# Performance work log

Measured on AMD Instinct MI355X. Metric: run time of the kernel, lower is better.

## Reference

```python
import jax, jax.numpy as jnp
import numpy as np

B, S, D = 2, 2048, 2048
HQ, HKV, HD = 16, 8, 128
F = 8192
V = 32000
L = 2
SW = 512
SOFTCAP = 50.0
THETA = 10000.0
EPS = 1e-6
LAYER_TYPES = ("sliding_attention", "full_attention")
SCALE = HD ** -0.5


def _rms_norm(x, w):
    # Gemma-style RMSNorm: fp32 compute, (1 + weight) scale
    x32 = x.astype(jnp.float32)
    n = x32 * jax.lax.rsqrt(jnp.mean(x32 * x32, axis=-1, keepdims=True) + EPS)
    return (n * (1.0 + w.astype(jnp.float32))).astype(x.dtype)


def _rotate_half(x):
    x1, x2 = jnp.split(x, 2, axis=-1)
    return jnp.concatenate([-x2, x1], axis=-1)


def _rope_cos_sin(position_ids):
    inv_freq = 1.0 / (THETA ** (jnp.arange(0, HD, 2, dtype=jnp.float32) / HD))  # [HD/2]
    freqs = position_ids.astype(jnp.float32)[..., None] * inv_freq  # [B,S,HD/2]
    emb = jnp.concatenate([freqs, freqs], axis=-1)  # [B,S,HD]
    return jnp.cos(emb), jnp.sin(emb)


def _apply_rope(q, k, cos, sin):
    # q,k: [B,H,S,HD]; cos,sin: [B,S,HD] -> unsqueeze head dim
    c, s = cos[:, None], sin[:, None]
    return q * c + _rotate_half(q) * s, k * c + _rotate_half(k) * s


def _build_masks(attention_mask, position_ids):
    key_mask = attention_mask.astype(bool)  # [B,S]
    # segment ids from position resets (packed sequences)
    boundaries = (position_ids[:, 1:] <= position_ids[:, :-1]).astype(jnp.int32)
    seg = jnp.cumsum(jnp.concatenate([jnp.ones((B, 1), jnp.int32), boundaries], axis=1), axis=1)
    block = seg[:, :, None] == seg[:, None, :]  # [B,S,S]
    full = (key_mask[:, None, :] & block)[:, None]  # [B,1,S,S]
    rows = jnp.arange(S)
    dist = rows[:, None] - rows[None, :]
    left = (SW + 1) // 2
    right = SW // 2 + 1
    window = ((dist >= 0) & (dist < left)) | ((dist < 0) & (-dist < right))
    sliding = full & window[None, None]
    return {"full_attention": full, "sliding_attention": sliding}


def _attention(x, l, wq, wk, wv, wo, q_norm_w, k_norm_w, cos, sin, mask):
    q = jnp.einsum("bsd,dhe->bhse", x, wq[l].reshape(D, HQ, HD))
    k = jnp.einsum("bsd,dhe->bhse", x, wk[l].reshape(D, HKV, HD))
    v = jnp.einsum("bsd,dhe->bhse", x, wv[l].reshape(D, HKV, HD))
    q = _rms_norm(q, q_norm_w[l])
    k = _rms_norm(k, k_norm_w[l])
    q, k = _apply_rope(q, k, cos, sin)
    rep = HQ // HKV
    k = jnp.repeat(k, rep, axis=1)  # repeat_kv
    v = jnp.repeat(v, rep, axis=1)
    scores = jnp.einsum("bhqd,bhkd->bhqk", q, k) * SCALE
    scores = jnp.tanh(scores / SOFTCAP) * SOFTCAP  # logit softcapping
    big_neg = jnp.finfo(jnp.float32).min
    scores = jnp.where(mask, scores, big_neg)
    probs = jax.nn.softmax(scores.astype(jnp.float32), axis=-1).astype(x.dtype)
    out = jnp.einsum("bhqk,bhkd->bhqd", probs, v)
    out = out.transpose(0, 2, 1, 3).reshape(B, S, HQ * HD)
    return out @ wo[l]


def _mlp(x, l, w_gate_up, w_down):
    gu = x @ w_gate_up[l]
    gate, up = jnp.split(gu, 2, axis=-1)
    return (jax.nn.gelu(gate, approximate=True) * up) @ w_down[l]


def setup_inputs() -> dict:
    key = jax.random.key(0)
    ks = jax.random.split(key, 12)
    w = lambda k, shape: (jax.random.normal(k, shape, jnp.float32) * 0.02)
    inp = {
        "embed": w(ks[0], (V, D)),
        "wq": w(ks[1], (L, D, HQ * HD)),
        "wk": w(ks[2], (L, D, HKV * HD)),
        "wv": w(ks[3], (L, D, HKV * HD)),
        "wo": w(ks[4], (L, HQ * HD, D)),
        "q_norm_w": jnp.zeros((L, HD), jnp.float32),
        "k_norm_w": jnp.zeros((L, HD), jnp.float32),
        "ln_in": jnp.zeros((L, D), jnp.float32),
        "ln_post_attn": jnp.zeros((L, D), jnp.float32),
        "ln_pre_ffn": jnp.zeros((L, D), jnp.float32),
        "ln_post_ffn": jnp.zeros((L, D), jnp.float32),
        "w_gate_up": w(ks[5], (L, D, 2 * F)),
        "w_down": w(ks[6], (L, F, D)),
        "final_norm_w": jnp.zeros((D,), jnp.float32),
        "input_ids": jax.random.randint(ks[7], (B, S), 0, V, jnp.int32),
        "attention_mask": jnp.ones((B, S), jnp.int32),
        # packed sequences: positions reset at the midpoint of each row
        "position_ids": jnp.broadcast_to(
            jnp.concatenate([jnp.arange(S // 2), jnp.arange(S - S // 2)]).astype(jnp.int32)[None, :],
            (B, S),
        ),
    }
    return inp


def reference(embed, wq, wk, wv, wo, q_norm_w, k_norm_w, ln_in, ln_post_attn,
              ln_pre_ffn, ln_post_ffn, w_gate_up, w_down, final_norm_w,
              input_ids, attention_mask, position_ids):
    masks = _build_masks(attention_mask, position_ids)
    cos, sin = _rope_cos_sin(position_ids)
    # scaled word embedding (Gemma style)
    x = embed[input_ids] * jnp.asarray(D ** 0.5, embed.dtype)
    for l in range(L):
        mask = masks[LAYER_TYPES[l]]
        h = _rms_norm(x, ln_in[l])
        h = _attention(h, l, wq, wk, wv, wo, q_norm_w, k_norm_w, cos, sin, mask)
        x = x + _rms_norm(h, ln_post_attn[l])
        h = _rms_norm(x, ln_pre_ffn[l])
        h = _mlp(h, l, w_gate_up, w_down)
        x = x + _rms_norm(h, ln_post_ffn[l])
    return _rms_norm(x, final_norm_w)
```

## Files before the change

### kernel.cpp

```cpp
#include <hip/hip_runtime.h>
#include <cstdint>
#include <cstddef>

typedef __bf16 bf16x8 __attribute__((ext_vector_type(8)));
typedef float  f32x4  __attribute__((ext_vector_type(4)));

#define BATCH 2
#define SEQ   2048
#define DMODEL 2048
#define NHQ   16
#define NHKV  8
#define HDIM  128
#define FFDIM 8192
#define NTOK  4096

__device__ __forceinline__ f32x4 mfma16(bf16x8 a, bf16x8 b, f32x4 c) {
    return __builtin_amdgcn_mfma_f32_16x16x32_bf16(a, b, c, 0, 0, 0);
}

__device__ __forceinline__ void gload16(const __bf16* g, __bf16* l) {
    __builtin_amdgcn_global_load_lds(
        (const __attribute__((address_space(1))) void*)g,
        (__attribute__((address_space(3))) void*)l, 16, 0, 0);
}

__device__ inline float wave_sum64(float v) {
    v += __shfl_xor(v, 1);  v += __shfl_xor(v, 2);  v += __shfl_xor(v, 4);
    v += __shfl_xor(v, 8);  v += __shfl_xor(v, 16); v += __shfl_xor(v, 32);
    return v;
}

__device__ inline float block_sum256(float v, float* lds4) {
    v = wave_sum64(v);
    const int w = threadIdx.x >> 6;
    __syncthreads();
    if ((threadIdx.x & 63) == 0) lds4[w] = v;
    __syncthreads();
    return lds4[0] + lds4[1] + lds4[2] + lds4[3];
}

__device__ __forceinline__ float softcap_exp(float s_raw) {
    const float K1 = 0.08838834764831845f * 0.04f;
    float u = __expf(s_raw * K1);
    return __expf(50.f - 100.f * __builtin_amdgcn_rcpf(1.f + u));
}

__global__ void transpose_cvt(const float* __restrict__ src, __bf16* __restrict__ dst,
                              int K, int N) {
    __shared__ float tile[32][33];
    const int tx = threadIdx.x, ty = threadIdx.y;
    const int n0 = blockIdx.x * 32, k0 = blockIdx.y * 32;
    #pragma unroll
    for (int i = 0; i < 4; ++i)
        tile[ty + i * 8][tx] = src[(size_t)(k0 + ty + i * 8) * N + n0 + tx];
    __syncthreads();
    #pragma unroll
    for (int i = 0; i < 4; ++i)
        dst[(size_t)(n0 + ty + i * 8) * K + k0 + tx] = (__bf16)tile[tx][ty + i * 8];
}

__global__ void transpose_cvt_gu(const float* __restrict__ src, __bf16* __restrict__ dst,
                                 int K, int N) {
    __shared__ float tile[32][33];
    const int tx = threadIdx.x, ty = threadIdx.y;
    const int n0 = blockIdx.x * 32, k0 = blockIdx.y * 32;
    #pragma unroll
    for (int i = 0; i < 4; ++i)
        tile[ty + i * 8][tx] = src[(size_t)(k0 + ty + i * 8) * N + n0 + tx];
    __syncthreads();
    #pragma unroll
    for (int i = 0; i < 4; ++i) {
        int n = n0 + ty + i * 8;
        int rI;
        if (n < 8192) rI = ((n & ~15) << 1) + (n & 15);
        else { int u = n - 8192; rI = ((u & ~15) << 1) + 16 + (u & 15); }
        dst[(size_t)rI * K + k0 + tx] = (__bf16)tile[tx][ty + i * 8];
    }
}

__global__ void transpose_bf16_k(const __bf16* __restrict__ src0, __bf16* __restrict__ dst0,
                                 int R, int C) {
    __shared__ __bf16 tile[32][34];
    const int z = blockIdx.z;
    const __bf16* src = src0 + (size_t)z * R * C;
    __bf16* dst = dst0 + (size_t)z * R * C;
    const int tx = threadIdx.x, ty = threadIdx.y;
    const int c0 = blockIdx.x * 32, r0 = blockIdx.y * 32;
    #pragma unroll
    for (int i = 0; i < 4; ++i)
        tile[ty + i * 8][tx] = src[(size_t)(r0 + ty + i * 8) * C + c0 + tx];
    __syncthreads();
    #pragma unroll
    for (int i = 0; i < 4; ++i)
        dst[(size_t)(c0 + ty + i * 8) * R + r0 + tx] = tile[tx][ty + i * 8];
}

__global__ __launch_bounds__(256) void embed_k(const float* __restrict__ emb,
                                               const int* __restrict__ ids,
                                               float* __restrict__ x) {
    const int row = blockIdx.x, t = threadIdx.x;
    const int id = ids[row];
    const size_t src = (size_t)id * DMODEL, dst = (size_t)row * DMODEL;
    const float sc = 45.2548339959390f;
    float4 a = *(const float4*)&emb[src + t * 4];
    float4 b = *(const float4*)&emb[src + t * 4 + 1024];
    a.x *= sc; a.y *= sc; a.z *= sc; a.w *= sc;
    b.x *= sc; b.y *= sc; b.z *= sc; b.w *= sc;
    *(float4*)&x[dst + t * 4] = a;
    *(float4*)&x[dst + t * 4 + 1024] = b;
}

__global__ __launch_bounds__(256) void seg_scan(const int* __restrict__ pos,
                                                int* __restrict__ seg) {
    __shared__ int wsum[4];
    const int b = blockIdx.x, t = threadIdx.x;
    const int lane = t & 63, wv = t >> 6;
    const int base = b * SEQ;
    int f[8]; int loc = 0;
    #pragma unroll
    for (int i = 0; i < 8; ++i) {
        int s = t * 8 + i;
        int fl = (s > 0) ? (pos[base + s] <= pos[base + s - 1]) : 0;
        f[i] = fl; loc += fl;
    }
    int sc = loc;
    for (int o = 1; o < 64; o <<= 1) { int n = __shfl_up(sc, o); if (lane >= o) sc += n; }
    if (lane == 63) wsum[wv] = sc;
    __syncthreads();
    int wb = 0;
    for (int i = 0; i < wv; ++i) wb += wsum[i];
    int run = wb + sc - loc + 1;
    #pragma unroll
    for (int i = 0; i < 8; ++i) { run += f[i]; seg[base + t * 8 + i] = run; }
}

template<int MODE, int NH>
__global__ __launch_bounds__(256) void fused_norm_k(
        float* __restrict__ x, const float* __restrict__ hA, const float* __restrict__ hB,
        const float* __restrict__ wA, const float* __restrict__ wB,
        __bf16* __restrict__ outb, float* __restrict__ outf) {
    __shared__ float lds4[4];
    const int row = blockIdx.x, t = threadIdx.x;
    const size_t base = (size_t)row * DMODEL;
    const int c0 = t * 4, c1 = t * 4 + 1024;
    float v[8];
    if constexpr (MODE == 0) {
        float4 a = *(const float4*)&x[base + c0];
        float4 b = *(const float4*)&x[base + c1];
        v[0]=a.x; v[1]=a.y; v[2]=a.z; v[3]=a.w;
        v[4]=b.x; v[5]=b.y; v[6]=b.z; v[7]=b.w;
    } else {
        float4 ha = *(const float4*)&hA[base + c0];
        float4 hb = *(const float4*)&hA[base + c1];
        float hv[8] = {ha.x, ha.y, ha.z, ha.w, hb.x, hb.y, hb.z, hb.w};
        if constexpr (NH == 2) {
            float4 ga = *(const float4*)&hB[base + c0];
            float4 gb = *(const float4*)&hB[base + c1];
            hv[0]+=ga.x; hv[1]+=ga.y; hv[2]+=ga.z; hv[3]+=ga.w;
            hv[4]+=gb.x; hv[5]+=gb.y; hv[6]+=gb.z; hv[7]+=gb.w;
        }
        float ss = 0.f;
        #pragma unroll
        for (int i = 0; i < 8; ++i) ss += hv[i] * hv[i];
        float tot = block_sum256(ss, lds4);
        float rs = rsqrtf(tot * (1.f / DMODEL) + 1e-6f);
        float4 xa = *(const float4*)&x[base + c0];
        float4 xb = *(const float4*)&x[base + c1];
        float xv[8] = {xa.x, xa.y, xa.z, xa.w, xb.x, xb.y, xb.z, xb.w};
        #pragma unroll
        for (int i = 0; i < 8; ++i) {
            int c = (i < 4) ? c0 + i : c1 + i - 4;
            v[i] = xv[i] + hv[i] * rs * (1.f + wA[c]);
        }
        float4 o0 = {v[0], v[1], v[2], v[3]}, o1 = {v[4], v[5], v[6], v[7]};
        *(float4*)&x[base + c0] = o0;
        *(float4*)&x[base + c1] = o1;
    }
    float ss2 = 0.f;
    #pragma unroll
    for (int i = 0; i < 8; ++i) ss2 += v[i] * v[i];
    float tot2 = block_sum256(ss2, lds4);
    float rs2 = rsqrtf(tot2 * (1.f / DMODEL) + 1e-6f);
    #pragma unroll
    for (int i = 0; i < 8; ++i) {
        int c = (i < 4) ? c0 + i : c1 + i - 4;
        float o = v[i] * rs2 * (1.f + wB[c]);
        if constexpr (MODE == 2) outf[base + c] = o;
        else outb[base + c] = (__bf16)o;
    }
}

template<int MH, int NH>
__device__ __forceinline__ void quad(f32x4 (&acc)[8][4], const bf16x8 (&af)[4][2],
                                     const bf16x8 (&bfr)[2][2]) {
    #pragma unroll
    for (int mq = 0; mq < 4; ++mq)
        #pragma unroll
        for (int nq = 0; nq < 2; ++nq)
            #pragma unroll
            for (int ks = 0; ks < 2; ++ks)
                acc[MH*4+mq][NH*2+nq] = mfma16(af[mq][ks], bfr[nq][ks], acc[MH*4+mq][NH*2+nq]);
}

template<typename OutT, int GELU>
__global__ __launch_bounds__(512, 2) void gemm8p(const __bf16* __restrict__ A,
                                                 const __bf16* __restrict__ Bw,
                                                 OutT* __restrict__ C,
                                                 int M, int N, int Ksub, int lda, int ldb) {
    __shared__ __bf16 lds[65536];
    const int z = blockIdx.z;
    A += (size_t)z * Ksub;
    Bw += (size_t)z * Ksub;
    C += (size_t)z * M * N;

    const int nx = gridDim.x;
    const int ny = gridDim.y;
    const int nwg = nx * ny;
    const int orig = blockIdx.y * nx + blockIdx.x;
    const int wg = ((nwg & 7) == 0) ? ((orig & 7) * (nwg >> 3) + (orig >> 3)) : orig;
    const int gsize = 8 * nx;
    const int gid = wg / gsize;
    const int first_m = gid * 8;
    const int rows = min(8, ny - first_m);
    const int loc = wg - gid * gsize;
    const int bm = (first_m + loc % rows) * 256;
    const int bn = (loc / rows) * 256;

    const int t = threadIdx.x;
    const int w = t >> 6, lane = t & 63;
    const int wm = w >> 2, wn = w & 3;
    const int lg = lane >> 4, lr = lane & 15;

    const int rS = t >> 3, sS = t & 7;
    const int colS = ((sS ^ (rS & 7)) << 3);
    const __bf16* Ag = A + (size_t)(bm + rS) * lda + colS;
    const __bf16* Bg = Bw + (size_t)(bn + rS) * ldb + colS;
    const int nt = Ksub >> 6;

#define STAGE_AU(kt, h, s) { \
        const __bf16* g_ = Ag + (size_t)((h) * 128 + (s) * 64) * lda + (size_t)(kt) * 64; \
        gload16(g_, &lds[(((kt) & 1) << 15) + (h) * 8192 + (s) * 4096 + t * 8]); }
#define STAGE_BU(kt, h, s) { \
        const __bf16* g_ = Bg + (size_t)((h) * 128 + (s) * 64) * ldb + (size_t)(kt) * 64; \
        gload16(g_, &lds[(((kt) & 1) << 15) + 16384 + (h) * 8192 + (s) * 4096 + t * 8]); }

    f32x4 acc[8][4] = {};
    bf16x8 af[4][2], bf0[2][2], bf1[2][2];

    const int swz = (lr & 7) << 3;
    const int aBase = wm * 8192;
    const int bBase = 16384 + (wn >> 1) * 8192;
    const int bRow0 = (wn & 1) * 64;
    const int lo0 = (lg * 8) ^ swz;
    const int lo1 = (32 + lg * 8) ^ swz;

#define RD_A(bufv, rowoff) { \
        _Pragma("unroll") \
        for (int mq = 0; mq < 4; ++mq) { \
            const int rb_ = (bufv) + aBase + ((rowoff) + mq * 16 + lr) * 64; \
            af[mq][0] = *(const bf16x8*)&lds[rb_ + lo0]; \
            af[mq][1] = *(const bf16x8*)&lds[rb_ + lo1]; } }
#define RD_B0(bufv) { \
        _Pragma("unroll") \
        for (int nq = 0; nq < 2; ++nq) { \
            const int rb_ = (bufv) + bBase + (bRow0 + nq * 16 + lr) * 64; \
            bf0[nq][0] = *(const bf16x8*)&lds[rb_ + lo0]; \
            bf0[nq][1] = *(const bf16x8*)&lds[rb_ + lo1]; } }
#define RD_B1(bufv) { \
        _Pragma("unroll") \
        for (int nq = 0; nq < 2; ++nq) { \
            const int rb_ = (bufv) + bBase + (bRow0 + 32 + nq * 16 + lr) * 64; \
            bf1[nq][0] = *(const bf16x8*)&lds[rb_ + lo0]; \
            bf1[nq][1] = *(const bf16x8*)&lds[rb_ + lo1]; } }

    STAGE_BU(0, 0, 0); STAGE_BU(0, 0, 1); STAGE_BU(0, 1, 0); STAGE_BU(0, 1, 1);
    STAGE_AU(0, 0, 0); STAGE_AU(0, 1, 0); STAGE_AU(0, 0, 1); STAGE_AU(0, 1, 1);

    for (int kt = 0; kt < nt; ++kt) {
        const int buf = (kt & 1) << 15;
        const bool p1 = (kt + 1 < nt);
        if (p1) {
            STAGE_BU(kt + 1, 0, 0); STAGE_BU(kt + 1, 0, 1);
            asm volatile("s_waitcnt vmcnt(4)" ::: "memory");
        } else {
            asm volatile("s_waitcnt vmcnt(2)" ::: "memory");
        }
        __builtin_amdgcn_s_barrier();
        asm volatile("" ::: "memory");
        RD_A(buf, 0); RD_B0(buf);
        asm volatile("s_waitcnt lgkmcnt(0)" ::: "memory");
        __builtin_amdgcn_sched_barrier(0);
        __builtin_amdgcn_s_setprio(1);
        quad<0,0>(acc, af, bf0);
        __builtin_amdgcn_s_setprio(0);
        asm volatile("" ::: "memory");
        if (p1) { STAGE_BU(kt + 1, 1, 0); STAGE_BU(kt + 1, 1, 1); }
        RD_B1(buf);
        asm volatile("s_waitcnt lgkmcnt(0)" ::: "memory");
        __builtin_amdgcn_sched_barrier(0);
        __builtin_amdgcn_s_setprio(1);
        quad<0,1>(acc, af, bf1);
        __builtin_amdgcn_s_setprio(0);
        asm volatile("" ::: "memory");
        if (p1) {
            STAGE_AU(kt + 1, 0, 0); STAGE_AU(kt + 1, 1, 0);
            asm volatile("s_waitcnt vmcnt(6)" ::: "memory");
        } else {
            asm volatile("s_waitcnt vmcnt(0)" ::: "memory");
        }
        __builtin_amdgcn_s_barrier();
        asm volatile("" ::: "memory");
        RD_A(buf, 64);
        asm volatile("s_waitcnt lgkmcnt(0)" ::: "memory");
        __builtin_amdgcn_sched_barrier(0);
        __builtin_amdgcn_s_setprio(1);
        quad<1,1>(acc, af, bf1);
        __builtin_amdgcn_s_setprio(0);
        asm volatile("" ::: "memory");
        if (p1) { STAGE_AU(kt + 1, 0, 1); STAGE_AU(kt + 1, 1, 1); }
        __builtin_amdgcn_sched_barrier(0);
        __builtin_amdgcn_s_setprio(1);
        quad<1,0>(acc, af, bf0);
        __builtin_amdgcn_s_setprio(0);
        asm volatile("" ::: "memory");
    }
#undef STAGE_AU
#undef STAGE_BU
#undef RD_A
#undef RD_B0
#undef RD_B1

    if constexpr (GELU) {
        const int nhalf = N >> 1;
        #pragma unroll
        for (int m = 0; m < 8; ++m)
            #pragma unroll
            for (int pp = 0; pp < 2; ++pp)
                #pragma unroll
                for (int r = 0; r < 4; ++r) {
                    float g = acc[m][2 * pp][r];
                    float u = acc[m][2 * pp + 1][r];
                    float a2 = 1.5957691216057308f * (g + 0.044715f * g * g * g);
                    float sig = __builtin_amdgcn_rcpf(1.f + __expf(-a2));
                    float res = g * sig * u;
                    const int row = bm + wm * 128 + m * 16 + lg * 4 + r;
                    const int col = (bn >> 1) + wn * 32 + pp * 16 + lr;
                    C[(size_t)row * nhalf + col] = (OutT)res;
                }
    } else {
        #pragma unroll
        for (int m = 0; m < 8; ++m)
            #pragma unroll
            for (int n = 0; n < 4; ++n)
                #pragma unroll
                for (int r = 0; r < 4; ++r) {
                    const int row = bm + wm * 128 + m * 16 + lg * 4 + r;
                    const int col = bn + wn * 64 + n * 16 + lr;
                    C[(size_t)row * N + col] = (OutT)acc[m][n][r];
                }
    }
}

__global__ __launch_bounds__(256) void qkv_post(const __bf16* __restrict__ qkv,
                                                const float* __restrict__ qnw,
                                                const float* __restrict__ knw,
                                                const int* __restrict__ posid,
                                                __bf16* __restrict__ qg,
                                                __bf16* __restrict__ kg,
                                                __bf16* __restrict__ vg) {
    const int slot = blockIdx.x * 4 + (threadIdx.x >> 6);
    const int lane = threadIdx.x & 63;
    const int token = slot >> 5, j = slot & 31;
    const int b = token >> 11, s = token & (SEQ - 1);
    int base;
    const float* nw = nullptr;
    if (j < 16)      { base = j * 128;                nw = qnw; }
    else if (j < 24) { base = 2048 + (j - 16) * 128;  nw = knw; }
    else             { base = 3072 + (j - 24) * 128; }
    float e0 = (float)qkv[(size_t)token * 4096 + base + lane];
    float e1 = (float)qkv[(size_t)token * 4096 + base + lane + 64];
    if (j < 24) {
        float ss = wave_sum64(e0 * e0 + e1 * e1);
        float rs = rsqrtf(ss * (1.f / 128.f) + 1e-6f);
        e0 *= rs * (1.f + nw[lane]);
        e1 *= rs * (1.f + nw[lane + 64]);
        float p = (float)posid[token];
        float inv = exp2f(-13.287712379549449f * ((float)lane * (1.f / 64.f)));
        float f = p * inv;
        float c = cosf(f), sn = sinf(f);
        float o0 = e0 * c - e1 * sn;
        float o1 = e1 * c + e0 * sn;
        e0 = o0; e1 = o1;
    }
    size_t dst; __bf16* out;
    if (j < 16)      { dst = ((size_t)(b * NHQ  + j)        * SEQ + s) * HDIM; out = qg; }
    else if (j < 24) { dst = ((size_t)(b * NHKV + (j - 16)) * SEQ + s) * HDIM; out = kg; }
    else             { dst = ((size_t)(b * NHKV + (j - 24)) * SEQ + s) * HDIM; out = vg; }
    out[dst + lane] = (__bf16)e0;
    out[dst + lane + 64] = (__bf16)e1;
}

template<int SLIDING>
__global__ __launch_bounds__(256, 2) void attn_k(const __bf16* __restrict__ qg,
                                                 const __bf16* __restrict__ kg,
                                                 const __bf16* __restrict__ vtg,
                                                 const int* __restrict__ seg,
                                                 const int* __restrict__ amask,
                                                 __bf16* __restrict__ outg) {
    __shared__ __align__(16) __bf16 Ks[64][136];
    __shared__ __align__(16) __bf16 Vs[128][72];
    __shared__ __align__(16) __bf16 Ps[4][16][72];
    __shared__ int segq_s[64], segk_s[64], kmk_s[64];
    __shared__ int flag_s;
    const int bh = blockIdx.y;
    const int b = bh >> 4, h = bh & 15, kvh = h >> 1;
    const int qb = blockIdx.x * 64;
    const int t = threadIdx.x, w = t >> 6, lane = t & 63;
    const int lg = lane >> 4, lr = lane & 15;
    const int segbase = b * SEQ;

    const size_t qoff = ((size_t)(b * NHQ + h) * SEQ + qb + w * 16) * HDIM;
    bf16x8 qf[4];
    #pragma unroll
    for (int kk = 0; kk < 4; ++kk)
        qf[kk] = *(const bf16x8*)&qg[qoff + (size_t)lr * HDIM + kk * 32 + lg * 8];
    if (t < 64) segq_s[t] = seg[segbase + qb + t];

    const int sqmin = seg[segbase + qb], sqmax = seg[segbase + qb + 63];

    const int krow = t >> 4, kcol = (t & 15) * 8;
    const int vrow = t >> 3, vcol = (t & 7) * 8;
    const __bf16* kB = kg + ((size_t)(b * NHKV + kvh) * SEQ) * HDIM + (size_t)krow * HDIM + kcol;
    const __bf16* vB = vtg + ((size_t)(b * NHKV + kvh) * HDIM + vrow) * SEQ + vcol;

    auto chunk_active = [&](int kb) -> bool {
        if (SLIDING && (qb - kb < -318 || qb - kb > 319)) return false;
        int skmin = seg[segbase + kb], skmax = seg[segbase + kb + 63];
        return (skmax >= sqmin) && (skmin <= sqmax);
    };
    auto next_kb = [&](int kb) -> int {
        for (kb += 64; kb < SEQ; kb += 64)
            if (chunk_active(kb)) return kb;
        return SEQ;
    };

    int4 kr0, kr1, kr2, kr3, vr0, vr1, vr2, vr3;
#define LOADR(kb_) { \
        kr0 = *(const int4*)(kB + (size_t)(kb_) * HDIM); \
        kr1 = *(const int4*)(kB + (size_t)((kb_) + 16) * HDIM); \
        kr2 = *(const int4*)(kB + (size_t)((kb_) + 32) * HDIM); \
        kr3 = *(const int4*)(kB + (size_t)((kb_) + 48) * HDIM); \
        vr0 = *(const int4*)(vB + (kb_)); \
        vr1 = *(const int4*)(vB + (size_t)32 * SEQ + (kb_)); \
        vr2 = *(const int4*)(vB + (size_t)64 * SEQ + (kb_)); \
        vr3 = *(const int4*)(vB + (size_t)96 * SEQ + (kb_)); }

    f32x4 oacc[8] = {};
    float den[4] = {0.f, 0.f, 0.f, 0.f};

    int kb = chunk_active(0) ? 0 : next_kb(0);
    if (kb < SEQ) LOADR(kb);

    while (kb < SEQ) {
        const int nkb = next_kb(kb);
        __syncthreads();
        *(int4*)&Ks[krow     ][kcol] = kr0;
        *(int4*)&Ks[krow + 16][kcol] = kr1;
        *(int4*)&Ks[krow + 32][kcol] = kr2;
        *(int4*)&Ks[krow + 48][kcol] = kr3;
        *(int4*)&Vs[vrow     ][vcol] = vr0;
        *(int4*)&Vs[vrow + 32][vcol] = vr1;
        *(int4*)&Vs[vrow + 64][vcol] = vr2;
        *(int4*)&Vs[vrow + 96][vcol] = vr3;
        if (w == 0) {
            int m = amask[segbase + kb + lane];
            int sk = seg[segbase + kb + lane];
            kmk_s[lane] = m; segk_s[lane] = sk;
            bool allm = (__ballot(m != 0) == ~0ull);
            bool segu = __all(sk == sqmin) && (sqmin == sqmax);
            bool wall = !SLIDING || (qb - kb >= -193 && qb - kb <= 192);
            if (lane == 0) flag_s = (allm && segu && wall) ? 1 : 0;
        }
        __syncthreads();
        if (nkb < SEQ) LOADR(nkb);
        const bool fast = (flag_s != 0);

        #pragma unroll
        for (int n = 0; n < 4; ++n) {
            f32x4 sc = {};
            #pragma unroll
            for (int kk = 0; kk < 4; ++kk) {
                bf16x8 bfr = *(const bf16x8*)&Ks[n * 16 + lr][kk * 32 + lg * 8];
                sc = mfma16(qf[kk], bfr, sc);
            }
            if (fast) {
                #pragma unroll
                for (int r = 0; r < 4; ++r) {
                    int row = lg * 4 + r;
                    float p = softcap_exp(sc[r]);
                    den[r] += p;
                    Ps[w][row][n * 16 + lr] = (__bf16)p;
                }
            } else {
                #pragma unroll
                for (int r = 0; r < 4; ++r) {
                    int row = lg * 4 + r;
                    int qi = qb + w * 16 + row;
                    int ki = kb + n * 16 + lr;
                    bool ok = (kmk_s[n * 16 + lr] != 0) &&
                              (segq_s[w * 16 + row] == segk_s[n * 16 + lr]);
                    if (SLIDING) { int d = qi - ki; ok = ok && (d >= -256) && (d <= 255); }
                    float p = ok ? softcap_exp(sc[r]) : 0.f;
                    den[r] += p;
                    Ps[w][row][n * 16 + lr] = (__bf16)p;
                }
            }
        }
        #pragma unroll
        for (int kk2 = 0; kk2 < 2; ++kk2) {
            bf16x8 pf = *(const bf16x8*)&Ps[w][lr][kk2 * 32 + lg * 8];
            #pragma unroll
            for (int n2 = 0; n2 < 8; ++n2) {
                bf16x8 vf = *(const bf16x8*)&Vs[n2 * 16 + lr][kk2 * 32 + lg * 8];
                oacc[n2] = mfma16(pf, vf, oacc[n2]);
            }
        }
        kb = nkb;
    }
#undef LOADR
    #pragma unroll
    for (int r = 0; r < 4; ++r) {
        float v = den[r];
        v += __shfl_xor(v, 1); v += __shfl_xor(v, 2);
        v += __shfl_xor(v, 4); v += __shfl_xor(v, 8);
        den[r] = __builtin_amdgcn_rcpf(v);
    }
    #pragma unroll
    for (int n2 = 0; n2 < 8; ++n2)
        #pragma unroll
        for (int r = 0; r < 4; ++r) {
            int row = qb + w * 16 + lg * 4 + r;
            float val = oacc[n2][r] * den[r];
            outg[((size_t)(b * SEQ) + row) * DMODEL + h * HDIM + n2 * 16 + lr] = (__bf16)val;
        }
}

extern "C" void kernel_launch(void* const* d_in, const int* in_sizes, int n_in,
                              void* d_out, int out_size, void* d_ws, size_t ws_size,
                              hipStream_t stream) {
    const float* embedw = (const float*)d_in[0];
    const float* wq   = (const float*)d_in[1];
    const float* wk   = (const float*)d_in[2];
    const float* wv   = (const float*)d_in[3];
    const float* wo   = (const float*)d_in[4];
    const float* qnw  = (const float*)d_in[5];
    const float* knw  = (const float*)d_in[6];
    const float* lnin = (const float*)d_in[7];
    const float* lnpa = (const float*)d_in[8];
    const float* lnpf = (const float*)d_in[9];
    const float* lnpff= (const float*)d_in[10];
    const float* wguW = (const float*)d_in[11];
    const float* wdnW = (const float*)d_in[12];
    const float* fnw  = (const float*)d_in[13];
    const int* ids    = (const int*)d_in[14];
    const int* amask  = (const int*)d_in[15];
    const int* posid  = (const int*)d_in[16];
    float* outp = (float*)d_out;

    char* ws = (char*)d_ws;
    size_t off = 0;
    auto A = [&](size_t b) -> char* {
        char* p = ws + off;
        off = (off + b + 255) & ~(size_t)255;
        return p;
    };
    __bf16* qkvwt = (__bf16*)A((size_t)4096 * 2048 * 2);
    __bf16* wot   = (__bf16*)A((size_t)2048 * 2048 * 2);
    __bf16* wgut  = (__bf16*)A((size_t)16384 * 2048 * 2);
    __bf16* wdnt  = (__bf16*)A((size_t)2048 * 8192 * 2);
    float*  x     = (float*)A((size_t)NTOK * DMODEL * 4);
    __bf16* hbuf  = (__bf16*)A((size_t)NTOK * DMODEL * 2);
    __bf16* qkvb  = (__bf16*)A((size_t)NTOK * 4096 * 2);
    __bf16* qbh   = (__bf16*)A((size_t)BATCH * NHQ  * SEQ * HDIM * 2);
    __bf16* kbh   = (__bf16*)A((size_t)BATCH * NHKV * SEQ * HDIM * 2);
    __bf16* vbh   = (__bf16*)A((size_t)BATCH * NHKV * SEQ * HDIM * 2);
    __bf16* vtbh  = (__bf16*)A((size_t)BATCH * NHKV * SEQ * HDIM * 2);
    __bf16* attnb = (__bf16*)A((size_t)NTOK * DMODEL * 2);
    __bf16* actb  = (__bf16*)A((size_t)NTOK * FFDIM * 2);
    float*  pbuf  = (float*)A((size_t)2 * NTOK * DMODEL * 4);
    int*    seg   = (int*)A((size_t)BATCH * SEQ * 4);
    if (off > ws_size) return;

    const dim3 tb(32, 8);
    seg_scan<<<BATCH, 256, 0, stream>>>(posid, seg);
    embed_k<<<NTOK, 256, 0, stream>>>(embedw, ids, x);
    fused_norm_k<0,1><<<NTOK, 256, 0, stream>>>(x, nullptr, nullptr, nullptr, lnin, hbuf, nullptr);

    for (int l = 0; l < 2; ++l) {
        transpose_cvt<<<dim3(64, 64), tb, 0, stream>>>(wq + (size_t)l * 2048 * 2048,
            qkvwt, 2048, 2048);
        transpose_cvt<<<dim3(32, 64), tb, 0, stream>>>(wk + (size_t)l * 2048 * 1024,
            qkvwt + (size_t)2048 * 2048, 2048, 1024);
        transpose_cvt<<<dim3(32, 64), tb, 0, stream>>>(wv + (size_t)l * 2048 * 1024,
            qkvwt + (size_t)3072 * 2048, 2048, 1024);
        transpose_cvt<<<dim3(64, 64), tb, 0, stream>>>(wo + (size_t)l * 2048 * 2048,
            wot, 2048, 2048);
        transpose_cvt_gu<<<dim3(512, 64), tb, 0, stream>>>(wguW + (size_t)l * 2048 * 16384,
            wgut, 2048, 16384);
        transpose_cvt<<<dim3(64, 256), tb, 0, stream>>>(wdnW + (size_t)l * 8192 * 2048,
            wdnt, 8192, 2048);

        gemm8p<__bf16,0><<<dim3(16, 16, 1), 512, 0, stream>>>(hbuf, qkvwt, qkvb,
                                                              4096, 4096, 2048, 2048, 2048);
        qkv_post<<<32768, 256, 0, stream>>>(qkvb, qnw + l * 128, knw + l * 128, posid,
                                            qbh, kbh, vbh);
        transpose_bf16_k<<<dim3(4, 64, BATCH * NHKV), tb, 0, stream>>>(vbh, vtbh, SEQ, HDIM);
        if (l == 0)
            attn_k<1><<<dim3(SEQ / 64, BATCH * NHQ), 256, 0, stream>>>(qbh, kbh, vtbh, seg,
                                                                       amask, attnb);
        else
            attn_k<0><<<dim3(SEQ / 64, BATCH * NHQ), 256, 0, stream>>>(qbh, kbh, vtbh, seg,
                                                                       amask, attnb);
        gemm8p<float,0><<<dim3(8, 16, 2), 512, 0, stream>>>(attnb, wot, pbuf,
                                                            4096, 2048, 1024, 2048, 2048);
        fused_norm_k<1,2><<<NTOK, 256, 0, stream>>>(x, pbuf, pbuf + (size_t)NTOK * DMODEL,
                                                    lnpa + l * 2048, lnpf + l * 2048,
                                                    hbuf, nullptr);
        gemm8p<__bf16,1><<<dim3(64, 16, 1), 512, 0, stream>>>(hbuf, wgut, actb,
                                                              4096, 16384, 2048, 2048, 2048);
        gemm8p<float,0><<<dim3(8, 16, 2), 512, 0, stream>>>(actb, wdnt, pbuf,
                                                            4096, 2048, 4096, 8192, 8192);
        if (l == 0)
            fused_norm_k<1,2><<<NTOK, 256, 0, stream>>>(x, pbuf, pbuf + (size_t)NTOK * DMODEL,
                                                        lnpff, lnin + 2048, hbuf, nullptr);
        else
            fused_norm_k<2,2><<<NTOK, 256, 0, stream>>>(x, pbuf, pbuf + (size_t)NTOK * DMODEL,
                                                        lnpff + 2048, fnw, nullptr, outp);
    }
}
```

Measured before the change: 1.419 ms.

## Store split-K GEMM partials in bf16, raise attention occupancy, add MFMA priority

The split-K output-projection and down-projection GEMMs now write their two partial sums as bf16 instead of fp32. The fused norm kernel is templated to read bf16 partials, which halves the partial-buffer traffic. Separately, the attention kernel's launch bounds go from 2 to 3 blocks per SIMD, and s_setprio brackets are placed around its MFMA loops. The bf16 partials lose precision before the residual add, and the tighter launch bound may force register spills.

```diff
diff --git a/kernel.cpp b/kernel.cpp
--- a/kernel.cpp
+++ b/kernel.cpp
@@ -3,6 +3,7 @@
 #include <cstddef>
 
 typedef __bf16 bf16x8 __attribute__((ext_vector_type(8)));
+typedef __bf16 bf16x4 __attribute__((ext_vector_type(4)));
 typedef float  f32x4  __attribute__((ext_vector_type(4)));
 
 #define BATCH 2
@@ -43,6 +44,15 @@
     const float K1 = 0.08838834764831845f * 0.04f;
     float u = __expf(s_raw * K1);
     return __expf(50.f - 100.f * __builtin_amdgcn_rcpf(1.f + u));
+}
+
+__device__ __forceinline__ void ld4f(const float* p, float v[4]) {
+    float4 a = *(const float4*)p;
+    v[0] = a.x; v[1] = a.y; v[2] = a.z; v[3] = a.w;
+}
+__device__ __forceinline__ void ld4f(const __bf16* p, float v[4]) {
+    bf16x4 a = *(const bf16x4*)p;
+    v[0] = (float)a[0]; v[1] = (float)a[1]; v[2] = (float)a[2]; v[3] = (float)a[3];
 }
 
 __global__ void transpose_cvt(const float* __restrict__ src, __bf16* __restrict__ dst,
@@ -134,9 +144,9 @@
     for (int i = 0; i < 8; ++i) { run += f[i]; seg[base + t * 8 + i] = run; }
 }
 
-template<int MODE, int NH>
+template<int MODE, int NH, typename HT>
 __global__ __launch_bounds__(256) void fused_norm_k(
-        float* __restrict__ x, const float* __restrict__ hA, const float* __restrict__ hB,
+        float* __restrict__ x, const HT* __restrict__ hA, const HT* __restrict__ hB,
         const float* __restrict__ wA, const float* __restrict__ wB,
         __bf16* __restrict__ outb, float* __restrict__ outf) {
     __shared__ float lds4[4];
@@ -150,14 +160,15 @@
         v[0]=a.x; v[1]=a.y; v[2]=a.z; v[3]=a.w;
         v[4]=b.x; v[5]=b.y; v[6]=b.z; v[7]=b.w;
     } else {
-        float4 ha = *(const float4*)&hA[base + c0];
-        float4 hb = *(const float4*)&hA[base + c1];
-        float hv[8] = {ha.x, ha.y, ha.z, ha.w, hb.x, hb.y, hb.z, hb.w};
+        float hv[8];
+        ld4f(hA + base + c0, &hv[0]);
+        ld4f(hA + base + c1, &hv[4]);
         if constexpr (NH == 2) {
-            float4 ga = *(const float4*)&hB[base + c0];
-            float4 gb = *(const float4*)&hB[base + c1];
-            hv[0]+=ga.x; hv[1]+=ga.y; hv[2]+=ga.z; hv[3]+=ga.w;
-            hv[4]+=gb.x; hv[5]+=gb.y; hv[6]+=gb.z; hv[7]+=gb.w;
+            float gv[8];
+            ld4f(hB + base + c0, &gv[0]);
+            ld4f(hB + base + c1, &gv[4]);
+            #pragma unroll
+            for (int i = 0; i < 8; ++i) hv[i] += gv[i];
         }
         float ss = 0.f;
         #pragma unroll
@@ -401,7 +412,7 @@
 }
 
 template<int SLIDING>
-__global__ __launch_bounds__(256, 2) void attn_k(const __bf16* __restrict__ qg,
+__global__ __launch_bounds__(256, 3) void attn_k(const __bf16* __restrict__ qg,
                                                  const __bf16* __restrict__ kg,
                                                  const __bf16* __restrict__ vtg,
                                                  const int* __restrict__ seg,
@@ -488,11 +499,13 @@
         #pragma unroll
         for (int n = 0; n < 4; ++n) {
             f32x4 sc = {};
+            __builtin_amdgcn_s_setprio(1);
             #pragma unroll
             for (int kk = 0; kk < 4; ++kk) {
                 bf16x8 bfr = *(const bf16x8*)&Ks[n * 16 + lr][kk * 32 + lg * 8];
                 sc = mfma16(qf[kk], bfr, sc);
             }
+            __builtin_amdgcn_s_setprio(0);
             if (fast) {
                 #pragma unroll
                 for (int r = 0; r < 4; ++r) {
@@ -516,6 +529,7 @@
                 }
             }
         }
+        __builtin_amdgcn_s_setprio(1);
         #pragma unroll
         for (int kk2 = 0; kk2 < 2; ++kk2) {
             bf16x8 pf = *(const bf16x8*)&Ps[w][lr][kk2 * 32 + lg * 8];
@@ -525,6 +539,7 @@
                 oacc[n2] = mfma16(pf, vf, oacc[n2]);
             }
         }
+        __builtin_amdgcn_s_setprio(0);
         kb = nkb;
     }
 #undef LOADR
@@ -587,14 +602,15 @@
     __bf16* vtbh  = (__bf16*)A((size_t)BATCH * NHKV * SEQ * HDIM * 2);
     __bf16* attnb = (__bf16*)A((size_t)NTOK * DMODEL * 2);
     __bf16* actb  = (__bf16*)A((size_t)NTOK * FFDIM * 2);
-    float*  pbuf  = (float*)A((size_t)2 * NTOK * DMODEL * 4);
+    __bf16* pbuf  = (__bf16*)A((size_t)2 * NTOK * DMODEL * 2);
     int*    seg   = (int*)A((size_t)BATCH * SEQ * 4);
     if (off > ws_size) return;
 
     const dim3 tb(32, 8);
     seg_scan<<<BATCH, 256, 0, stream>>>(posid, seg);
     embed_k<<<NTOK, 256, 0, stream>>>(embedw, ids, x);
-    fused_norm_k<0,1><<<NTOK, 256, 0, stream>>>(x, nullptr, nullptr, nullptr, lnin, hbuf, nullptr);
+    fused_norm_k<0,1,float><<<NTOK, 256, 0, stream>>>(x, nullptr, nullptr, nullptr, lnin,
+                                                      hbuf, nullptr);
 
     for (int l = 0; l < 2; ++l) {
         transpose_cvt<<<dim3(64, 64), tb, 0, stream>>>(wq + (size_t)l * 2048 * 2048,
@@ -621,20 +637,25 @@
         else
             attn_k<0><<<dim3(SEQ / 64, BATCH * NHQ), 256, 0, stream>>>(qbh, kbh, vtbh, seg,
                                                                        amask, attnb);
-        gemm8p<float,0><<<dim3(8, 16, 2), 512, 0, stream>>>(attnb, wot, pbuf,
-                                                            4096, 2048, 1024, 2048, 2048);
-        fused_norm_k<1,2><<<NTOK, 256, 0, stream>>>(x, pbuf, pbuf + (size_t)NTOK * DMODEL,
-                                                    lnpa + l * 2048, lnpf + l * 2048,
-                                                    hbuf, nullptr);
+        gemm8p<__bf16,0><<<dim3(8, 16, 2), 512, 0, stream>>>(attnb, wot, pbuf,
+                                                             4096, 2048, 1024, 2048, 2048);
+        fused_norm_k<1,2,__bf16><<<NTOK, 256, 0, stream>>>(x, pbuf,
+                                                           pbuf + (size_t)NTOK * DMODEL,
+                                                           lnpa + l * 2048, lnpf + l * 2048,
+                                                           hbuf, nullptr);
         gemm8p<__bf16,1><<<dim3(64, 16, 1), 512, 0, stream>>>(hbuf, wgut, actb,
                                                               4096, 16384, 2048, 2048, 2048);
-        gemm8p<float,0><<<dim3(8, 16, 2), 512, 0, stream>>>(actb, wdnt, pbuf,
-                                                            4096, 2048, 4096, 8192, 8192);
+        gemm8p<__bf16,0><<<dim3(8, 16, 2), 512, 0, stream>>>(actb, wdnt, pbuf,
+                                                             4096, 2048, 4096, 8192, 8192);
         if (l == 0)
-            fused_norm_k<1,2><<<NTOK, 256, 0, stream>>>(x, pbuf, pbuf + (size_t)NTOK * DMODEL,
-                                                        lnpff, lnin + 2048, hbuf, nullptr);
+            fused_norm_k<1,2,__bf16><<<NTOK, 256, 0, stream>>>(x, pbuf,
+                                                               pbuf + (size_t)NTOK * DMODEL,
+                                                               lnpff, lnin + 2048,
+                                                               hbuf, nullptr);
         else
-            fused_norm_k<2,2><<<NTOK, 256, 0, stream>>>(x, pbuf, pbuf + (size_t)NTOK * DMODEL,
-                                                        lnpff + 2048, fnw, nullptr, outp);
-    }
-}
+            fused_norm_k<2,2,__bf16><<<NTOK, 256, 0, stream>>>(x, pbuf,
+                                                               pbuf + (size_t)NTOK * DMODEL,
+                                                               lnpff + 2048, fnw,
+                                                               nullptr, outp);
+    }
+}
```

Result: no change. 1.396 ms (-1.6%).
